# Performance work log

Measured on AMD Instinct MI355X. Metric: run time of the kernel, lower is better.

The kernel has to match this reference:

```python
import jax, jax.numpy as jnp
import numpy as np

RES = 256
RANK = 12
OUT = 8
INIT = 0.01


def _sample_plane(plane, xy):
    """Bilinear grid_sample, align_corners=False, padding_mode='border'.

    plane: [H, W, rank]; xy: [N, 2] with xy[:,0]=x (indexes W), xy[:,1]=y (indexes H).
    Returns [N, rank].
    """
    H, W = plane.shape[0], plane.shape[1]
    # unnormalize (align_corners=False): ix = ((x+1)*W - 1)/2, then border-clamp
    ix = jnp.clip((xy[:, 0] + 1.0) * (W * 0.5) - 0.5, 0.0, W - 1.0)
    iy = jnp.clip((xy[:, 1] + 1.0) * (H * 0.5) - 0.5, 0.0, H - 1.0)
    x0 = jnp.floor(ix)
    y0 = jnp.floor(iy)
    wx = (ix - x0)[:, None]
    wy = (iy - y0)[:, None]
    x0i = x0.astype(jnp.int32)
    y0i = y0.astype(jnp.int32)
    x1i = jnp.minimum(x0i + 1, W - 1)
    y1i = jnp.minimum(y0i + 1, H - 1)
    v00 = plane[y0i, x0i]  # [N, rank]
    v01 = plane[y0i, x1i]
    v10 = plane[y1i, x0i]
    v11 = plane[y1i, x1i]
    top = v00 + wx * (v01 - v00)
    bot = v10 + wx * (v11 - v10)
    return top + wy * (bot - top)


def setup_inputs() -> dict:
    key = jax.random.key(0)
    k1, k2, k3, k4, k5 = jax.random.split(key, 5)
    N = 2_000_000
    coordinates = jax.random.uniform(k1, (N, 3), jnp.float32, -1.0, 1.0)
    plane_xy = jax.random.normal(k2, (RES, RES, RANK), jnp.float32) * INIT
    plane_xz = jax.random.normal(k3, (RES, RES, RANK), jnp.float32) * INIT
    plane_yz = jax.random.normal(k4, (RES, RES, RANK), jnp.float32) * INIT
    proj_w = jax.random.normal(k5, (OUT, 3 * RANK), jnp.float32) * INIT
    proj_b = jnp.zeros((OUT,), jnp.float32)
    return {"coordinates": coordinates, "plane_xy": plane_xy, "plane_xz": plane_xz,
            "plane_yz": plane_yz, "proj_w": proj_w, "proj_b": proj_b}


def reference(coordinates, plane_xy, plane_xz, plane_yz, proj_w, proj_b):
    c = jnp.clip(coordinates, -1.0, 1.0)
    xy_feat = _sample_plane(plane_xy, c[:, (0, 1)])
    xz_feat = _sample_plane(plane_xz, c[:, (0, 2)])
    yz_feat = _sample_plane(plane_yz, c[:, (1, 2)])
    triplane = jnp.concatenate([xy_feat, xz_feat, yz_feat], axis=1)  # [N, 3*rank]
    out = triplane @ proj_w.T + proj_b
    return jnp.clip(out, -10.0, 10.0)
```

## Files before the change

kernel.cpp:

```cpp
#include <hip/hip_runtime.h>

#define RES   256
#define RANK  12
#define NOUT  8
#define NPLANE (RES * RES)

typedef _Float16 half8 __attribute__((ext_vector_type(8)));
typedef _Float16 h2    __attribute__((ext_vector_type(2)));
typedef int      i32x4 __attribute__((ext_vector_type(4)));
typedef float    f32x4 __attribute__((ext_vector_type(4)));

__global__ __launch_bounds__(256) void project_planes_kernel(
    const float* __restrict__ pxy, const float* __restrict__ pxz,
    const float* __restrict__ pyz, const float* __restrict__ w,
    half8* __restrict__ P)
{
    int tid = blockIdx.x * 256 + threadIdx.x;
    int p = tid >> 16;
    int t = tid & (NPLANE - 1);
    const float* plane = (p == 0) ? pxy : ((p == 1) ? pxz : pyz);

    const float4* src = (const float4*)(plane + (size_t)t * RANK);
    float4 a = src[0], b = src[1], c = src[2];
    float v[RANK] = {a.x, a.y, a.z, a.w, b.x, b.y, b.z, b.w, c.x, c.y, c.z, c.w};

    half8 h;
#pragma unroll
    for (int k = 0; k < NOUT; ++k) {
        const float* wr = w + k * (3 * RANK) + p * RANK;
        float s = 0.0f;
#pragma unroll
        for (int r = 0; r < RANK; ++r) s = fmaf(wr[r], v[r], s);
        h[k] = (_Float16)s;
    }
    P[tid] = h;
}

__device__ __forceinline__ void unnorm(float c, int& i0, float& fr)
{
    float ic = fminf(fmaxf(fmaf(c, 128.0f, 127.5f), 0.0f), (float)(RES - 1));
    float f = floorf(ic);
    fr = ic - f;
    i0 = (int)f;
}

__device__ __forceinline__ void sample_col(
    const half8* __restrict__ base, int wi, float wf, int hi, float hf,
    int xs, half8& acc)
{
    int cx = min(wi + xs, RES - 1);
    float wx = xs ? wf : (1.0f - wf);
    int r0 = hi << 8;
    int r1 = min(hi + 1, RES - 1) << 8;
    half8 t0 = base[r0 + cx];
    half8 t1 = base[r1 + cx];
    _Float16 wa = (_Float16)(wx * (1.0f - hf));
    _Float16 wb = (_Float16)(wx * hf);
    acc += t0 * wa + t1 * wb;
}

__global__ __launch_bounds__(256) void triplane_gather_pair_kernel(
    const float* __restrict__ coords, const half8* __restrict__ P,
    const float* __restrict__ bias, float* __restrict__ out, int N)
{
    int g = blockIdx.x * 256 + threadIdx.x;
    int p = g >> 1;
    int xs = g & 1;
    if (p >= N) return;

    float x = __builtin_nontemporal_load(coords + 3 * p + 0);
    float y = __builtin_nontemporal_load(coords + 3 * p + 1);
    float z = __builtin_nontemporal_load(coords + 3 * p + 2);

    int xi, yi, zi;
    float xf, yf, zf;
    unnorm(x, xi, xf);
    unnorm(y, yi, yf);
    unnorm(z, zi, zf);

    half8 acc = {};
    sample_col(P,              xi, xf, yi, yf, xs, acc);
    sample_col(P + NPLANE,     xi, xf, zi, zf, xs, acc);
    sample_col(P + 2 * NPLANE, yi, yf, zi, zf, xs, acc);

    i32x4 ai = __builtin_bit_cast(i32x4, acc);
    i32x4 bi;
    bi[0] = __shfl_xor(ai[0], 1);
    bi[1] = __shfl_xor(ai[1], 1);
    bi[2] = __shfl_xor(ai[2], 1);
    bi[3] = __shfl_xor(ai[3], 1);
    acc += __builtin_bit_cast(half8, bi);

    i32x4 s = __builtin_bit_cast(i32x4, acc);
    int u0 = xs ? s[2] : s[0];
    int u1 = xs ? s[3] : s[1];
    h2 c01 = __builtin_bit_cast(h2, u0);
    h2 c23 = __builtin_bit_cast(h2, u1);

    const f32x4* b4 = (const f32x4*)bias;
    f32x4 bb = b4[xs];
    f32x4 r;
    r.x = fminf(fmaxf((float)c01[0] + bb.x, -10.f), 10.f);
    r.y = fminf(fmaxf((float)c01[1] + bb.y, -10.f), 10.f);
    r.z = fminf(fmaxf((float)c23[0] + bb.z, -10.f), 10.f);
    r.w = fminf(fmaxf((float)c23[1] + bb.w, -10.f), 10.f);

    __builtin_nontemporal_store(r, (f32x4*)out + g);
}

__device__ __forceinline__ void sample12(const float* __restrict__ plane,
                                         float u, float v, float* __restrict__ f)
{
    float ix = fminf(fmaxf((u + 1.0f) * (RES * 0.5f) - 0.5f, 0.0f), RES - 1.0f);
    float iy = fminf(fmaxf((v + 1.0f) * (RES * 0.5f) - 0.5f, 0.0f), RES - 1.0f);
    float fx = floorf(ix), fy = floorf(iy);
    float wx = ix - fx, wy = iy - fy;
    int x0 = (int)fx, y0 = (int)fy;
    int x1 = min(x0 + 1, RES - 1), y1 = min(y0 + 1, RES - 1);
    float w00 = (1.0f - wx) * (1.0f - wy);
    float w01 = wx * (1.0f - wy);
    float w10 = (1.0f - wx) * wy;
    float w11 = wx * wy;
    const float4* p4 = (const float4*)plane;
    int i00 = (y0 * RES + x0) * 3, i01 = (y0 * RES + x1) * 3;
    int i10 = (y1 * RES + x0) * 3, i11 = (y1 * RES + x1) * 3;
#pragma unroll
    for (int j = 0; j < 3; ++j) {
        float4 c00 = p4[i00 + j], c01 = p4[i01 + j];
        float4 c10 = p4[i10 + j], c11 = p4[i11 + j];
        f[4 * j + 0] = fmaf(w00, c00.x, fmaf(w01, c01.x, fmaf(w10, c10.x, w11 * c11.x)));
        f[4 * j + 1] = fmaf(w00, c00.y, fmaf(w01, c01.y, fmaf(w10, c10.y, w11 * c11.y)));
        f[4 * j + 2] = fmaf(w00, c00.z, fmaf(w01, c01.z, fmaf(w10, c10.z, w11 * c11.z)));
        f[4 * j + 3] = fmaf(w00, c00.w, fmaf(w01, c01.w, fmaf(w10, c10.w, w11 * c11.w)));
    }
}

__global__ __launch_bounds__(256) void triplane_direct_kernel(
    const float* __restrict__ coords,
    const float* __restrict__ pxy, const float* __restrict__ pxz,
    const float* __restrict__ pyz,
    const float* __restrict__ w, const float* __restrict__ bias,
    float* __restrict__ out, int N)
{
    int i = blockIdx.x * 256 + threadIdx.x;
    if (i >= N) return;
    float x = coords[3 * i + 0];
    float y = coords[3 * i + 1];
    float z = coords[3 * i + 2];
    float f[3 * RANK];
    sample12(pxy, x, y, f + 0);
    sample12(pxz, x, z, f + RANK);
    sample12(pyz, y, z, f + 2 * RANK);
    float o[NOUT];
#pragma unroll
    for (int k = 0; k < NOUT; ++k) {
        const float* wr = w + k * (3 * RANK);
        float s = bias[k];
#pragma unroll
        for (int j = 0; j < 3 * RANK; ++j) s = fmaf(wr[j], f[j], s);
        o[k] = fminf(fmaxf(s, -10.f), 10.f);
    }
    float4* o4 = (float4*)(out + (size_t)i * NOUT);
    o4[0] = make_float4(o[0], o[1], o[2], o[3]);
    o4[1] = make_float4(o[4], o[5], o[6], o[7]);
}

extern "C" void kernel_launch(void* const* d_in, const int* in_sizes, int n_in,
                              void* d_out, int out_size, void* d_ws, size_t ws_size,
                              hipStream_t stream)
{
    const float* coords = (const float*)d_in[0];
    const float* pxy    = (const float*)d_in[1];
    const float* pxz    = (const float*)d_in[2];
    const float* pyz    = (const float*)d_in[3];
    const float* w      = (const float*)d_in[4];
    const float* b      = (const float*)d_in[5];
    float* out = (float*)d_out;
    int N = in_sizes[0] / 3;

    size_t needP = (size_t)3 * NPLANE * NOUT * sizeof(_Float16);
    if (ws_size >= needP) {
        half8* P = (half8*)d_ws;
        project_planes_kernel<<<(3 * NPLANE) / 256, 256, 0, stream>>>(pxy, pxz, pyz, w, P);
        long long threads = 2LL * N;
        int blocks = (int)((threads + 255) / 256);
        triplane_gather_pair_kernel<<<blocks, 256, 0, stream>>>(coords, P, b, out, N);
    } else {
        int blocks = (N + 255) / 256;
        triplane_direct_kernel<<<blocks, 256, 0, stream>>>(coords, pxy, pxz, pyz, w, b, out, N);
    }
}
```

Baseline: 155.3 us.

## Quantize projected planes to int8 with per-plane scale and fetch texel pairs in one load

Replaces the fp16 projected-plane table with an int8 table whose scale per plane comes from a max-abs reduction pass (atomicMax into slots). Each gather thread now reads two horizontally adjacent texels with a single 16-byte load rather than two 16-byte loads, handling the right-edge clamp by shifting the base index. The table shrinks by half, so more of it stays cache-resident and gather traffic drops. The cost is an extra projection pass, a memset, and int8 quantization error that may exceed the output tolerance.

```diff
diff --git a/kernel.cpp b/kernel.cpp
--- a/kernel.cpp
+++ b/kernel.cpp
@@ -5,35 +5,72 @@
 #define NOUT  8
 #define NPLANE (RES * RES)
 
-typedef _Float16 half8 __attribute__((ext_vector_type(8)));
-typedef _Float16 h2    __attribute__((ext_vector_type(2)));
-typedef int      i32x4 __attribute__((ext_vector_type(4)));
 typedef float    f32x4 __attribute__((ext_vector_type(4)));
-
-__global__ __launch_bounds__(256) void project_planes_kernel(
-    const float* __restrict__ pxy, const float* __restrict__ pxz,
+typedef unsigned u32x2 __attribute__((ext_vector_type(2)));
+
+#define PQ_BYTES  ((size_t)3 * NPLANE * NOUT)
+#define SLOT_OFF  PQ_BYTES
+
+__device__ __forceinline__ void project_texel(
+    int tid, const float* __restrict__ pxy, const float* __restrict__ pxz,
     const float* __restrict__ pyz, const float* __restrict__ w,
-    half8* __restrict__ P)
-{
-    int tid = blockIdx.x * 256 + threadIdx.x;
-    int p = tid >> 16;
+    int& p, float* __restrict__ o)
+{
+    p = tid >> 16;
     int t = tid & (NPLANE - 1);
     const float* plane = (p == 0) ? pxy : ((p == 1) ? pxz : pyz);
-
     const float4* src = (const float4*)(plane + (size_t)t * RANK);
     float4 a = src[0], b = src[1], c = src[2];
     float v[RANK] = {a.x, a.y, a.z, a.w, b.x, b.y, b.z, b.w, c.x, c.y, c.z, c.w};
-
-    half8 h;
 #pragma unroll
     for (int k = 0; k < NOUT; ++k) {
         const float* wr = w + k * (3 * RANK) + p * RANK;
         float s = 0.0f;
 #pragma unroll
         for (int r = 0; r < RANK; ++r) s = fmaf(wr[r], v[r], s);
-        h[k] = (_Float16)s;
-    }
-    P[tid] = h;
+        o[k] = s;
+    }
+}
+
+__global__ __launch_bounds__(256) void project_max_kernel(
+    const float* __restrict__ pxy, const float* __restrict__ pxz,
+    const float* __restrict__ pyz, const float* __restrict__ w,
+    unsigned* __restrict__ slots)
+{
+    int tid = blockIdx.x * 256 + threadIdx.x;
+    int p; float o[NOUT];
+    project_texel(tid, pxy, pxz, pyz, w, p, o);
+    float m = 0.0f;
+#pragma unroll
+    for (int k = 0; k < NOUT; ++k) m = fmaxf(m, fabsf(o[k]));
+#pragma unroll
+    for (int s = 1; s < 64; s <<= 1) m = fmaxf(m, __shfl_xor(m, s));
+    if ((threadIdx.x & 63) == 0) atomicMax(slots + p, __float_as_uint(m));
+}
+
+__global__ __launch_bounds__(256) void project_quant_kernel(
+    const float* __restrict__ pxy, const float* __restrict__ pxz,
+    const float* __restrict__ pyz, const float* __restrict__ w,
+    const unsigned* __restrict__ slots, u32x2* __restrict__ Pq)
+{
+    int tid = blockIdx.x * 256 + threadIdx.x;
+    int p; float o[NOUT];
+    project_texel(tid, pxy, pxz, pyz, w, p, o);
+    float mx = __uint_as_float(slots[p]);
+    float inv = mx > 0.0f ? 127.0f / mx : 0.0f;
+    unsigned q[NOUT];
+#pragma unroll
+    for (int k = 0; k < NOUT; ++k)
+        q[k] = (unsigned)(__float2int_rn(o[k] * inv) + 128);
+    u32x2 d;
+    d.x = q[0] | (q[1] << 8) | (q[2] << 16) | (q[3] << 24);
+    d.y = q[4] | (q[5] << 8) | (q[6] << 16) | (q[7] << 24);
+    Pq[tid] = d;
+}
+
+__device__ __forceinline__ float ub(unsigned v, int b)
+{
+    return (float)((v >> (8 * b)) & 0xffu);
 }
 
 __device__ __forceinline__ void unnorm(float c, int& i0, float& fr)
@@ -44,28 +81,14 @@
     i0 = (int)f;
 }
 
-__device__ __forceinline__ void sample_col(
-    const half8* __restrict__ base, int wi, float wf, int hi, float hf,
-    int xs, half8& acc)
-{
-    int cx = min(wi + xs, RES - 1);
-    float wx = xs ? wf : (1.0f - wf);
-    int r0 = hi << 8;
-    int r1 = min(hi + 1, RES - 1) << 8;
-    half8 t0 = base[r0 + cx];
-    half8 t1 = base[r1 + cx];
-    _Float16 wa = (_Float16)(wx * (1.0f - hf));
-    _Float16 wb = (_Float16)(wx * hf);
-    acc += t0 * wa + t1 * wb;
-}
-
-__global__ __launch_bounds__(256) void triplane_gather_pair_kernel(
-    const float* __restrict__ coords, const half8* __restrict__ P,
-    const float* __restrict__ bias, float* __restrict__ out, int N)
+__global__ __launch_bounds__(256) void triplane_gather_i8_kernel(
+    const float* __restrict__ coords, const unsigned char* __restrict__ Pq,
+    const unsigned* __restrict__ slots, const float* __restrict__ bias,
+    float* __restrict__ out, int N)
 {
     int g = blockIdx.x * 256 + threadIdx.x;
     int p = g >> 1;
-    int xs = g & 1;
+    int r = g & 1;
     if (p >= N) return;
 
     float x = __builtin_nontemporal_load(coords + 3 * p + 0);
@@ -78,34 +101,55 @@
     unnorm(y, yi, yf);
     unnorm(z, zi, zf);
 
-    half8 acc = {};
-    sample_col(P,              xi, xf, yi, yf, xs, acc);
-    sample_col(P + NPLANE,     xi, xf, zi, zf, xs, acc);
-    sample_col(P + 2 * NPLANE, yi, yf, zi, zf, xs, acc);
-
-    i32x4 ai = __builtin_bit_cast(i32x4, acc);
-    i32x4 bi;
-    bi[0] = __shfl_xor(ai[0], 1);
-    bi[1] = __shfl_xor(ai[1], 1);
-    bi[2] = __shfl_xor(ai[2], 1);
-    bi[3] = __shfl_xor(ai[3], 1);
-    acc += __builtin_bit_cast(half8, bi);
-
-    i32x4 s = __builtin_bit_cast(i32x4, acc);
-    int u0 = xs ? s[2] : s[0];
-    int u1 = xs ? s[3] : s[1];
-    h2 c01 = __builtin_bit_cast(h2, u0);
-    h2 c23 = __builtin_bit_cast(h2, u1);
+    float sc0 = __uint_as_float(slots[0]) * (1.0f / 127.0f);
+    float sc1 = __uint_as_float(slots[1]) * (1.0f / 127.0f);
+    float sc2 = __uint_as_float(slots[2]) * (1.0f / 127.0f);
+
+    float acc[NOUT];
+#pragma unroll
+    for (int k = 0; k < NOUT; ++k) acc[k] = 0.0f;
+    float ksub = 0.0f;
+
+#pragma unroll
+    for (int pl = 0; pl < 3; ++pl) {
+        int   wi = (pl == 2) ? yi : xi;
+        float wf = (pl == 2) ? yf : xf;
+        int   hi = (pl == 0) ? yi : zi;
+        float hf = (pl == 0) ? yf : zf;
+        float sc = (pl == 0) ? sc0 : ((pl == 1) ? sc1 : sc2);
+
+        int row = r ? min(hi + 1, RES - 1) : hi;
+        float wr = r ? hf : (1.0f - hf);
+        int b = min(wi, RES - 2);
+        float lo_w = (wi <= RES - 2) ? (1.0f - wf) : 0.0f;
+        float hi_w = (wi <= RES - 2) ? wf : 1.0f;
+        float el = wr * lo_w * sc;
+        float eh = wr * hi_w * sc;
+        ksub += 128.0f * (el + eh);
+
+        const uint4* addr = (const uint4*)(Pq + (size_t)pl * NPLANE * NOUT
+                                              + ((size_t)row << 11) + ((size_t)b << 3));
+        uint4 d = *addr;
+#pragma unroll
+        for (int c = 0; c < 4; ++c) {
+            acc[c]     = fmaf(el, ub(d.x, c), fmaf(eh, ub(d.z, c), acc[c]));
+            acc[c + 4] = fmaf(el, ub(d.y, c), fmaf(eh, ub(d.w, c), acc[c + 4]));
+        }
+    }
+#pragma unroll
+    for (int k = 0; k < NOUT; ++k) acc[k] -= ksub;
+
+#pragma unroll
+    for (int k = 0; k < NOUT; ++k) acc[k] += __shfl_xor(acc[k], 1);
 
     const f32x4* b4 = (const f32x4*)bias;
-    f32x4 bb = b4[xs];
-    f32x4 r;
-    r.x = fminf(fmaxf((float)c01[0] + bb.x, -10.f), 10.f);
-    r.y = fminf(fmaxf((float)c01[1] + bb.y, -10.f), 10.f);
-    r.z = fminf(fmaxf((float)c23[0] + bb.z, -10.f), 10.f);
-    r.w = fminf(fmaxf((float)c23[1] + bb.w, -10.f), 10.f);
-
-    __builtin_nontemporal_store(r, (f32x4*)out + g);
+    f32x4 bb = b4[r];
+    f32x4 o;
+    o.x = fminf(fmaxf((r ? acc[4] : acc[0]) + bb.x, -10.f), 10.f);
+    o.y = fminf(fmaxf((r ? acc[5] : acc[1]) + bb.y, -10.f), 10.f);
+    o.z = fminf(fmaxf((r ? acc[6] : acc[2]) + bb.z, -10.f), 10.f);
+    o.w = fminf(fmaxf((r ? acc[7] : acc[3]) + bb.w, -10.f), 10.f);
+    __builtin_nontemporal_store(o, (f32x4*)out + g);
 }
 
 __device__ __forceinline__ void sample12(const float* __restrict__ plane,
@@ -178,15 +222,22 @@
     float* out = (float*)d_out;
     int N = in_sizes[0] / 3;
 
-    size_t needP = (size_t)3 * NPLANE * NOUT * sizeof(_Float16);
-    if (ws_size >= needP) {
-        half8* P = (half8*)d_ws;
-        project_planes_kernel<<<(3 * NPLANE) / 256, 256, 0, stream>>>(pxy, pxz, pyz, w, P);
+    size_t need = PQ_BYTES + 12;
+    if (ws_size >= need) {
+        unsigned char* Pq = (unsigned char*)d_ws;
+        unsigned* slots = (unsigned*)(Pq + SLOT_OFF);
+        hipMemsetAsync(slots, 0, 12, stream);
+        project_max_kernel<<<(3 * NPLANE) / 256, 256, 0, stream>>>(
+            pxy, pxz, pyz, w, slots);
+        project_quant_kernel<<<(3 * NPLANE) / 256, 256, 0, stream>>>(
+            pxy, pxz, pyz, w, slots, (u32x2*)Pq);
         long long threads = 2LL * N;
         int blocks = (int)((threads + 255) / 256);
-        triplane_gather_pair_kernel<<<blocks, 256, 0, stream>>>(coords, P, b, out, N);
+        triplane_gather_i8_kernel<<<blocks, 256, 0, stream>>>(
+            coords, Pq, slots, b, out, N);
     } else {
         int blocks = (N + 255) / 256;
-        triplane_direct_kernel<<<blocks, 256, 0, stream>>>(coords, pxy, pxz, pyz, w, b, out, N);
-    }
-}
+        triplane_direct_kernel<<<blocks, 256, 0, stream>>>(
+            coords, pxy, pxz, pyz, w, b, out, N);
+    }
+}
```

After: 191.8 us. +23.6%, slower.
